# Kernel tuning notes

Hardware: AMD Instinct MI355X
Metric: run time of the kernel (lower is better)

## Reference

```python
import jax, jax.numpy as jnp
import numpy as np

N = 100000
E = 1600000
D_IN, D_EMB, D_OUT = 16, 128, 2


def _mlp(x, W1, b1, W2, b2):
    return jax.nn.relu(x @ W1 + b1) @ W2 + b2


def _gcn(x, edge_index, edge_weight, W, b):
    # PyG GCNConv: x' = W x, symmetric norm with self-loops (weight 1), scatter-add, + bias
    n = x.shape[0]
    x = x @ W
    row, col = edge_index[0], edge_index[1]
    deg = jax.ops.segment_sum(edge_weight, col, num_segments=n) + 1.0  # +1 for self-loop
    dis = jax.lax.rsqrt(deg)
    norm = dis[row] * edge_weight * dis[col]                      # [E]
    agg = jax.ops.segment_sum(norm[:, None] * x[row], col, num_segments=n)
    agg = agg + (dis * dis)[:, None] * x                          # self-loop contribution
    return agg + b


def setup_inputs() -> dict:
    key = jax.random.key(0)
    ks = jax.random.split(key, 16)
    s_in = 1.0 / np.sqrt(D_IN)
    s_emb = 1.0 / np.sqrt(D_EMB)
    return {
        "x": jax.random.normal(ks[0], (N, D_IN), dtype=jnp.float32),
        "edge_index": jax.random.randint(ks[1], (2, E), 0, N, dtype=jnp.int64),
        "edge_weight": jax.random.uniform(ks[2], (E,), dtype=jnp.float32),
        # encoder MLP
        "enc_W1": jax.random.normal(ks[3], (D_IN, D_EMB), dtype=jnp.float32) * s_in,
        "enc_b1": jnp.zeros((D_EMB,), jnp.float32),
        "enc_W2": jax.random.normal(ks[4], (D_EMB, D_EMB), dtype=jnp.float32) * s_emb,
        "enc_b2": jnp.zeros((D_EMB,), jnp.float32),
        # conv1 / conv2
        "c1_W": jax.random.normal(ks[5], (D_EMB, D_EMB), dtype=jnp.float32) * s_emb,
        "c1_b": jnp.zeros((D_EMB,), jnp.float32),
        "c2_W": jax.random.normal(ks[6], (D_EMB, D_EMB), dtype=jnp.float32) * s_emb,
        "c2_b": jnp.zeros((D_EMB,), jnp.float32),
        # decoder MLP
        "dec_W1": jax.random.normal(ks[7], (D_EMB, D_EMB), dtype=jnp.float32) * s_emb,
        "dec_b1": jnp.zeros((D_EMB,), jnp.float32),
        "dec_W2": jax.random.normal(ks[8], (D_EMB, D_OUT), dtype=jnp.float32) * s_emb,
        "dec_b2": jnp.zeros((D_OUT,), jnp.float32),
    }


def reference(x, edge_index, edge_weight,
              enc_W1, enc_b1, enc_W2, enc_b2,
              c1_W, c1_b, c2_W, c2_b,
              dec_W1, dec_b1, dec_W2, dec_b2):
    h = _mlp(x, enc_W1, enc_b1, enc_W2, enc_b2)
    h = jax.nn.relu(_gcn(h, edge_index, edge_weight, c1_W, c1_b))
    h = jax.nn.relu(_gcn(h, edge_index, edge_weight, c2_W, c2_b))
    h = _mlp(h, dec_W1, dec_b1, dec_W2, dec_b2)
    return jax.nn.softmax(h, axis=1)
```

## Files before the change

kernel.cpp:

```cpp
#include <hip/hip_runtime.h>

#define N_NODES 100000
#define N_EDGES 1600000
#define NBKT 391
#define BKT_CAP 4608
#define PART_BLOCKS 391

typedef _Float16 half8 __attribute__((ext_vector_type(8)));
typedef float floatx4 __attribute__((ext_vector_type(4)));


__global__ __launch_bounds__(256) void k_part(const int* __restrict__ ei,
                                              const float* __restrict__ ew,
                                              unsigned* __restrict__ cursor,
                                              unsigned* __restrict__ partA,
                                              float* __restrict__ partB) {
    __shared__ unsigned hist[NBKT];
    __shared__ unsigned lrank[NBKT];
    __shared__ unsigned basebuf[NBKT];
    int tid = threadIdx.x;
    int e0 = blockIdx.x * 4096 + tid * 16;
    for (int i = tid; i < NBKT; i += 256) { hist[i] = 0; lrank[i] = 0; }
    __syncthreads();

    unsigned bk[16];
    bool full = (e0 + 16 <= N_EDGES);
    if (full) {
        #pragma unroll
        for (int v = 0; v < 4; v++) {
            int4 c = *(const int4*)(ei + N_EDGES + e0 + v * 4);
            bk[v * 4 + 0] = (unsigned)c.x >> 8;
            bk[v * 4 + 1] = (unsigned)c.y >> 8;
            bk[v * 4 + 2] = (unsigned)c.z >> 8;
            bk[v * 4 + 3] = (unsigned)c.w >> 8;
        }
        #pragma unroll
        for (int i = 0; i < 16; i++) atomicAdd(&hist[bk[i]], 1u);
    } else {
        for (int i = 0; i < 16; i++) {
            if (e0 + i < N_EDGES) {
                bk[i] = (unsigned)ei[N_EDGES + e0 + i] >> 8;
                atomicAdd(&hist[bk[i]], 1u);
            }
        }
    }
    __syncthreads();
    for (int b = tid; b < NBKT; b += 256) {
        unsigned h = hist[b];
        basebuf[b] = h ? atomicAdd(&cursor[b], h) : 0u;
    }
    __syncthreads();

    if (full) {
        #pragma unroll
        for (int v = 0; v < 4; v++) {
            int4 c = *(const int4*)(ei + N_EDGES + e0 + v * 4);
            int4 r = *(const int4*)(ei + e0 + v * 4);
            float4 w = *(const float4*)(ew + e0 + v * 4);
            int cols[4] = {c.x, c.y, c.z, c.w};
            int rows[4] = {r.x, r.y, r.z, r.w};
            float ws4[4] = {w.x, w.y, w.z, w.w};
            #pragma unroll
            for (int i = 0; i < 4; i++) {
                unsigned b = bk[v * 4 + i];
                unsigned rk = atomicAdd(&lrank[b], 1u);
                size_t idx = (size_t)b * BKT_CAP + basebuf[b] + rk;
                partA[idx] = (((unsigned)cols[i] & 255u) << 17) | (unsigned)rows[i];
                partB[idx] = ws4[i];
            }
        }
    } else {
        for (int i = 0; i < 16; i++) {
            if (e0 + i < N_EDGES) {
                int col = ei[N_EDGES + e0 + i];
                int row = ei[e0 + i];
                float wv = ew[e0 + i];
                unsigned b = bk[i];
                unsigned rk = atomicAdd(&lrank[b], 1u);
                size_t idx = (size_t)b * BKT_CAP + basebuf[b] + rk;
                partA[idx] = (((unsigned)col & 255u) << 17) | (unsigned)row;
                partB[idx] = wv;
            }
        }
    }
}

__global__ __launch_bounds__(256) void k_stats(const unsigned* __restrict__ cursor,
                                               const unsigned* __restrict__ partA,
                                               const float* __restrict__ partB,
                                               float* __restrict__ dis,
                                               int* __restrict__ offs,
                                               int* __restrict__ cnt) {
    __shared__ unsigned hist[256];
    __shared__ unsigned sc[256];
    __shared__ float dacc[256];
    int tid = threadIdx.x;
    int j = blockIdx.x;
    int count = (int)cursor[j];
    size_t p0 = (size_t)j * BKT_CAP;
    hist[tid] = 0;
    dacc[tid] = 0.f;
    __syncthreads();
    for (int i = tid; i < count; i += 256) {
        unsigned a = partA[p0 + i];
        float w = partB[p0 + i];
        unsigned cl = (a >> 17) & 255u;
        atomicAdd(&hist[cl], 1u);
        atomicAdd(&dacc[cl], w);
    }
    __syncthreads();
    unsigned myc = hist[tid];
    sc[tid] = myc;
    __syncthreads();
    #pragma unroll
    for (int d = 1; d < 256; d <<= 1) {
        unsigned t = (tid >= d) ? sc[tid - d] : 0u;
        __syncthreads();
        sc[tid] += t;
        __syncthreads();
    }
    int col = j * 256 + tid;
    if (col < N_NODES) {
        dis[col] = rsqrtf(dacc[tid] + 1.0f);
        cnt[col] = (int)myc;
        offs[col] = (int)(p0 + (sc[tid] - myc));
    }
}

__global__ __launch_bounds__(256) void k_scatter(const unsigned* __restrict__ cursor,
                                                 const unsigned* __restrict__ partA,
                                                 const float* __restrict__ partB,
                                                 const int* __restrict__ offs,
                                                 const float* __restrict__ dis,
                                                 unsigned* __restrict__ csr,
                                                 float* __restrict__ svec) {
    __shared__ unsigned cur[256];
    __shared__ float sacc[256];
    int tid = threadIdx.x;
    int j = blockIdx.x;
    int count = (int)cursor[j];
    size_t p0 = (size_t)j * BKT_CAP;
    int col = j * 256 + tid;
    cur[tid] = (col < N_NODES) ? (unsigned)(offs[col] - (int)p0) : 0u;
    sacc[tid] = 0.f;
    __syncthreads();
    for (int i = tid; i < count; i += 256) {
        unsigned a = partA[p0 + i];
        float wv = partB[p0 + i];
        unsigned cl = (a >> 17) & 255u;
        unsigned row = a & 0x1FFFFu;
        unsigned r = atomicAdd(&cur[cl], 1u);
        int colg = j * 256 + (int)cl;
        float w = dis[row] * wv * dis[colg];
        _Float16 hw = (_Float16)w;
        unsigned short hb;
        __builtin_memcpy(&hb, &hw, 2);
        csr[p0 + r] = ((unsigned)hb << 17) | row;
        atomicAdd(&sacc[cl], (float)hw);
    }
    __syncthreads();
    if (col < N_NODES) {
        float d = dis[col];
        svec[col] = sacc[tid] + d * d;
    }
}

__global__ __launch_bounds__(256) void prep_mm(const float* __restrict__ W2,
                                               const float* __restrict__ c1W,
                                               _Float16* __restrict__ Wt0) {
    __shared__ float sW[128 * 128];
    int t = threadIdx.x;
    for (int i = t; i < 4096; i += 256) ((float4*)sW)[i] = ((const float4*)c1W)[i];
    __syncthreads();
    int k = blockIdx.x * 2 + (t >> 7);
    int col = t & 127;
    float acc = 0.f;
    #pragma unroll 8
    for (int j = 0; j < 128; j++) acc = fmaf(W2[k * 128 + j], sW[j * 128 + col], acc);
    Wt0[col * 128 + k] = (_Float16)acc;
}

__global__ __launch_bounds__(128) void prep_bb(const float* __restrict__ b2,
                                               const float* __restrict__ c1W,
                                               float* __restrict__ bb) {
    int c = threadIdx.x;
    float acc = 0.f;
    for (int j = 0; j < 128; j++) acc = fmaf(b2[j], c1W[j * 128 + c], acc);
    bb[c] = acc;
}

__global__ __launch_bounds__(256) void prep_tr(const float* __restrict__ Wa,
                                               const float* __restrict__ Wb,
                                               _Float16* __restrict__ Wt) {
    int m = blockIdx.x >> 4;
    const float* W = (m == 0) ? Wa : Wb;
    _Float16* o = Wt + (m + 1) * 16384;
    int base = (blockIdx.x & 15) * 1024 + threadIdx.x * 4;
    int col = base >> 7;
    int k0 = base & 127;
    #pragma unroll
    for (int i = 0; i < 4; i++) o[base + i] = (_Float16)W[(k0 + i) * 128 + col];
}


__global__ __launch_bounds__(256) void enc1_kernel(const float* __restrict__ x,
                                                   const float* __restrict__ W1,
                                                   const float* __restrict__ b1,
                                                   _Float16* __restrict__ out) {
    __shared__ float sX[256 * 17];
    __shared__ float sW[2048];
    __shared__ float sb[128];
    int t = threadIdx.x;
    int base = blockIdx.x * 256;
    for (int i = t; i < 512; i += 256) ((float4*)sW)[i] = ((const float4*)W1)[i];
    if (t < 128) sb[t] = b1[t];
    #pragma unroll
    for (int i = 0; i < 4; i++) {
        int f = i * 1024 + t * 4;
        int row = f >> 4, k = f & 15;
        float4 v = make_float4(0.f, 0.f, 0.f, 0.f);
        if (base + row < N_NODES) v = *(const float4*)(x + (size_t)(base + row) * 16 + k);
        *(float4*)(sX + row * 17 + k) = v;
    }
    __syncthreads();
    int row = base + t;
    if (row >= N_NODES) return;
    float xr[16];
    #pragma unroll
    for (int k = 0; k < 16; k++) xr[k] = sX[t * 17 + k];
    #pragma unroll 4
    for (int cb = 0; cb < 16; cb++) {
        float acc[8];
        #pragma unroll
        for (int jj = 0; jj < 8; jj++) acc[jj] = sb[cb * 8 + jj];
        #pragma unroll
        for (int k = 0; k < 16; k++) {
            float xv = xr[k];
            #pragma unroll
            for (int jj = 0; jj < 8; jj++) acc[jj] = fmaf(xv, sW[k * 128 + cb * 8 + jj], acc[jj]);
        }
        half8 h;
        #pragma unroll
        for (int jj = 0; jj < 8; jj++) h[jj] = (_Float16)fmaxf(acc[jj], 0.f);
        *(half8*)(out + (size_t)row * 128 + cb * 8) = h;
    }
}


#define GEMM_GRID 522

template <bool BIAS, bool RELU, bool DEC, bool SB>
__global__ __launch_bounds__(256, 2) void gemm_mfma(const _Float16* __restrict__ A,
                                                    const _Float16* __restrict__ Wt,
                                                    const float* __restrict__ bias,
                                                    _Float16* __restrict__ C,
                                                    const float* __restrict__ W2,
                                                    const float* __restrict__ b2,
                                                    float* __restrict__ sm_out,
                                                    const float* __restrict__ svec,
                                                    const float* __restrict__ bbv) {
    __shared__ _Float16 sA[2 * 64 * 128];
    __shared__ _Float16 sE[DEC ? 64 : 64 * 128];
    __shared__ float sW2[DEC ? 256 : 1];
    int t = threadIdx.x;
    int lane = t & 63;
    int w = t >> 6;
    int l15 = lane & 15;
    int l4 = lane >> 4;

    half8 bfrag[8][4];
    #pragma unroll
    for (int n = 0; n < 8; n++)
        #pragma unroll
        for (int kk = 0; kk < 4; kk++)
            bfrag[n][kk] = *(const half8*)(Wt + (n * 16 + l15) * 128 + kk * 32 + l4 * 8);

    float bcol[8];
    if constexpr (BIAS) {
        #pragma unroll
        for (int n = 0; n < 8; n++) bcol[n] = bias[n * 16 + l15];
    }
    float bbcol[8];
    if constexpr (SB) {
        #pragma unroll
        for (int n = 0; n < 8; n++) bbcol[n] = bbv[n * 16 + l15];
    }
    float b20 = 0.f, b21 = 0.f;
    if constexpr (DEC) {
        if (t < 256) sW2[t] = W2[t];
        b20 = b2[0]; b21 = b2[1];
    }

    auto STAGE = [&](int buf, int tile) {
        const _Float16* Ag = A + (size_t)tile * 64 * 128;
        #pragma unroll
        for (int i = 0; i < 4; i++) {
            int c = i * 256 + t;
            int row = c >> 4;
            int g = (c & 15) ^ (row & 7);
            const _Float16* src = Ag + row * 128 + g * 8;
            __builtin_amdgcn_global_load_lds(
                (const __attribute__((address_space(1))) void*)src,
                (__attribute__((address_space(3))) void*)(sA + buf * 8192 + (size_t)(i * 256 + w * 64) * 8),
                16, 0, 0);
        }
    };

    const int NT = (N_NODES + 63) / 64;
    int cur = 0;
    STAGE(0, blockIdx.x);

    for (int tile = blockIdx.x; tile < NT; tile += GEMM_GRID) {
        int nx = tile + GEMM_GRID;
        if (nx < NT) {
            STAGE(cur ^ 1, nx);
            asm volatile("s_waitcnt vmcnt(4)" ::: "memory");
        } else {
            asm volatile("s_waitcnt vmcnt(0)" ::: "memory");
        }
        __builtin_amdgcn_s_barrier();
        asm volatile("" ::: "memory");

        const _Float16* sAc = sA + cur * 8192;

        floatx4 acc[8];
        #pragma unroll
        for (int n = 0; n < 8; n++) acc[n] = (floatx4)(0.f);

        #pragma unroll
        for (int kk = 0; kk < 4; kk++) {
            int rloc = w * 16 + l15;
            int cl = kk * 4 + l4;
            int s = cl ^ (rloc & 7);
            half8 af = *(const half8*)(sAc + rloc * 128 + s * 8);
            #pragma unroll
            for (int n = 0; n < 8; n++)
                acc[n] = __builtin_amdgcn_mfma_f32_16x16x32_f16(af, bfrag[n][kk], acc[n], 0, 0, 0);
        }

        size_t base_row = (size_t)tile * 64;
        float s4[4];
        if constexpr (SB) {
            #pragma unroll
            for (int r = 0; r < 4; r++) {
                int rr = (int)base_row + w * 16 + l4 * 4 + r;
                s4[r] = (rr < N_NODES) ? svec[rr] : 0.f;
            }
        }
        if constexpr (DEC) {
            #pragma unroll
            for (int r = 0; r < 4; r++) {
                float p0 = 0.f, p1 = 0.f;
                #pragma unroll
                for (int n = 0; n < 8; n++) {
                    float v = acc[n][r];
                    if constexpr (BIAS) v += bcol[n];
                    if constexpr (RELU) v = fmaxf(v, 0.f);
                    int ch = n * 16 + l15;
                    p0 = fmaf(v, sW2[ch * 2 + 0], p0);
                    p1 = fmaf(v, sW2[ch * 2 + 1], p1);
                }
                #pragma unroll
                for (int m = 1; m < 16; m <<= 1) {
                    p0 += __shfl_xor(p0, m, 64);
                    p1 += __shfl_xor(p1, m, 64);
                }
                size_t grow = base_row + w * 16 + l4 * 4 + r;
                if (l15 == 0 && grow < N_NODES) {
                    float z0 = p0 + b20, z1 = p1 + b21;
                    float mx = fmaxf(z0, z1);
                    float e0 = expf(z0 - mx), e1 = expf(z1 - mx);
                    float si = 1.f / (e0 + e1);
                    *(float2*)(sm_out + grow * 2) = make_float2(e0 * si, e1 * si);
                }
            }
            __builtin_amdgcn_s_barrier();
            asm volatile("" ::: "memory");
        } else {
            #pragma unroll
            for (int n = 0; n < 8; n++) {
                #pragma unroll
                for (int r = 0; r < 4; r++) {
                    float v = acc[n][r];
                    if constexpr (SB) v += s4[r] * bbcol[n];
                    if constexpr (BIAS) v += bcol[n];
                    if constexpr (RELU) v = fmaxf(v, 0.f);
                    int row = w * 16 + l4 * 4 + r;
                    sE[row * 128 + n * 16 + l15] = (_Float16)v;
                }
            }
            __builtin_amdgcn_s_barrier();
            asm volatile("" ::: "memory");
            #pragma unroll
            for (int i = 0; i < 4; i++) {
                int c = i * 256 + t;
                int row = c >> 4;
                if (base_row + row < N_NODES) {
                    *(float4*)((char*)C + (base_row + row) * 256 + (c & 15) * 16) =
                        *(const float4*)((const char*)sE + (size_t)c * 16);
                }
            }
        }
        cur ^= 1;
    }
}


__global__ __launch_bounds__(256) void agg_kernel(const _Float16* __restrict__ m,
                                                  const int* __restrict__ offs,
                                                  const int* __restrict__ cnt,
                                                  const unsigned* __restrict__ csr,
                                                  const float* __restrict__ dis,
                                                  _Float16* __restrict__ out) {
    int wave = threadIdx.x >> 6;
    int lane = threadIdx.x & 63;
    int g = lane >> 4;
    int q = lane & 15;
    int j = blockIdx.x * 4 + wave;
    if (j >= N_NODES) return;
    int s = offs[j];
    int num = cnt[j];

    float acc[8];
    if (g == 0) {
        float d = dis[j];
        float dd = d * d;
        half8 mv = *(const half8*)(m + (size_t)j * 128 + q * 8);
        #pragma unroll
        for (int i = 0; i < 8; i++) acc[i] = dd * (float)mv[i];
    } else {
        #pragma unroll
        for (int i = 0; i < 8; i++) acc[i] = 0.f;
    }

    int e = 0;
    for (; e + 16 <= num; e += 16) {
        unsigned u0 = csr[s + e + g];
        unsigned u1 = csr[s + e + 4 + g];
        unsigned u2 = csr[s + e + 8 + g];
        unsigned u3 = csr[s + e + 12 + g];
        half8 r0 = *(const half8*)(m + (size_t)(u0 & 0x1FFFF) * 128 + q * 8);
        half8 r1 = *(const half8*)(m + (size_t)(u1 & 0x1FFFF) * 128 + q * 8);
        half8 r2 = *(const half8*)(m + (size_t)(u2 & 0x1FFFF) * 128 + q * 8);
        half8 r3 = *(const half8*)(m + (size_t)(u3 & 0x1FFFF) * 128 + q * 8);
        unsigned short b0 = (unsigned short)(u0 >> 17), b1 = (unsigned short)(u1 >> 17);
        unsigned short b2 = (unsigned short)(u2 >> 17), b3 = (unsigned short)(u3 >> 17);
        _Float16 h0, h1, h2, h3;
        __builtin_memcpy(&h0, &b0, 2); __builtin_memcpy(&h1, &b1, 2);
        __builtin_memcpy(&h2, &b2, 2); __builtin_memcpy(&h3, &b3, 2);
        float w0 = (float)h0, w1 = (float)h1, w2 = (float)h2, w3 = (float)h3;
        #pragma unroll
        for (int i = 0; i < 8; i++) acc[i] = fmaf(w0, (float)r0[i], acc[i]);
        #pragma unroll
        for (int i = 0; i < 8; i++) acc[i] = fmaf(w1, (float)r1[i], acc[i]);
        #pragma unroll
        for (int i = 0; i < 8; i++) acc[i] = fmaf(w2, (float)r2[i], acc[i]);
        #pragma unroll
        for (int i = 0; i < 8; i++) acc[i] = fmaf(w3, (float)r3[i], acc[i]);
    }
    for (; e < num; e += 4) {
        if (e + g < num) {
            unsigned u0 = csr[s + e + g];
            unsigned short b0 = (unsigned short)(u0 >> 17);
            _Float16 h0;
            __builtin_memcpy(&h0, &b0, 2);
            half8 r0 = *(const half8*)(m + (size_t)(u0 & 0x1FFFF) * 128 + q * 8);
            float w0 = (float)h0;
            #pragma unroll
            for (int i = 0; i < 8; i++) acc[i] = fmaf(w0, (float)r0[i], acc[i]);
        }
    }

    #pragma unroll
    for (int i = 0; i < 8; i++) {
        acc[i] += __shfl_xor(acc[i], 16, 64);
        acc[i] += __shfl_xor(acc[i], 32, 64);
    }

    if (g == 0) {
        half8 o;
        #pragma unroll
        for (int i = 0; i < 8; i++) o[i] = (_Float16)acc[i];
        *(half8*)(out + (size_t)j * 128 + q * 8) = o;
    }
}


extern "C" void kernel_launch(void* const* d_in, const int* in_sizes, int n_in,
                              void* d_out, int out_size, void* d_ws, size_t ws_size,
                              hipStream_t stream) {
    const float* x      = (const float*)d_in[0];
    const int*   ei     = (const int*)d_in[1];
    const float* ew     = (const float*)d_in[2];
    const float* enc_W1 = (const float*)d_in[3];
    const float* enc_b1 = (const float*)d_in[4];
    const float* enc_W2 = (const float*)d_in[5];
    const float* enc_b2 = (const float*)d_in[6];
    const float* c1_W   = (const float*)d_in[7];
    const float* c1_b   = (const float*)d_in[8];
    const float* c2_W   = (const float*)d_in[9];
    const float* c2_b   = (const float*)d_in[10];
    const float* dec_W1 = (const float*)d_in[11];
    const float* dec_b1 = (const float*)d_in[12];
    const float* dec_W2 = (const float*)d_in[13];
    const float* dec_b2 = (const float*)d_in[14];
    float* out = (float*)d_out;

    char* ws = (char*)d_ws;
    unsigned* partA = (unsigned*)(ws);
    float*    partB = (float*)(ws + 7206912);
    _Float16* B1 = (_Float16*)(ws);
    _Float16* B2 = (_Float16*)(ws + 25600000);
    _Float16* Wt = (_Float16*)(ws + 51200000);
    unsigned* cursor = (unsigned*)(ws + 51331072);
    float* dis     = (float*)(ws + 51333120);
    int*   offs    = (int*)  (ws + 51733120);
    int*   cnt     = (int*)  (ws + 52133120);
    unsigned* csr  = (unsigned*)(ws + 52533120);
    float* svec    = (float*)(ws + 59740032);
    float* bb      = (float*)(ws + 60140032);

    hipMemsetAsync(cursor, 0, 2048, stream);

    k_part<<<PART_BLOCKS, 256, 0, stream>>>(ei, ew, cursor, partA, partB);
    k_stats<<<NBKT, 256, 0, stream>>>(cursor, partA, partB, dis, offs, cnt);
    k_scatter<<<NBKT, 256, 0, stream>>>(cursor, partA, partB, offs, dis, csr, svec);

    prep_mm<<<64, 256, 0, stream>>>(enc_W2, c1_W, Wt);
    prep_bb<<<1, 128, 0, stream>>>(enc_b2, c1_W, bb);
    prep_tr<<<32, 256, 0, stream>>>(c2_W, dec_W1, Wt);
    enc1_kernel<<<(N_NODES + 255) / 256, 256, 0, stream>>>(x, enc_W1, enc_b1, B1);

    agg_kernel<<<N_NODES / 4, 256, 0, stream>>>(B1, offs, cnt, csr, dis, B2);
    gemm_mfma<true, true, false, true><<<GEMM_GRID, 256, 0, stream>>>(
        B2, Wt + 0 * 16384, c1_b, B1, nullptr, nullptr, nullptr, svec, bb);
    agg_kernel<<<N_NODES / 4, 256, 0, stream>>>(B1, offs, cnt, csr, dis, B2);
    gemm_mfma<true, true, false, false><<<GEMM_GRID, 256, 0, stream>>>(
        B2, Wt + 1 * 16384, c2_b, B1, nullptr, nullptr, nullptr, nullptr, nullptr);
    gemm_mfma<true, true, true, false><<<GEMM_GRID, 256, 0, stream>>>(
        B1, Wt + 2 * 16384, dec_b1, nullptr, dec_W2, dec_b2, out, nullptr, nullptr);
}
```

Measured before the change: 375.7 us.

## Retune partition and GEMM grid sizes and streamline aggregation gather loop

The partition kernel now processes half as many edges per block and launches twice as many blocks. The GEMM kernels take their tile stride from gridDim and are launched with larger grids, one of them giving each block a single tile, which spreads work over more blocks at the cost of less double-buffer prefetch reuse. The aggregation kernel drops its unrolled main loop plus remainder loop in favour of one predicated loop that clamps indices and zeroes weights for out-of-range edges. It also uses 32-bit shift/or addressing to cut index arithmetic.

```diff
diff --git a/kernel.cpp b/kernel.cpp
--- a/kernel.cpp
+++ b/kernel.cpp
@@ -4,7 +4,7 @@
 #define N_EDGES 1600000
 #define NBKT 391
 #define BKT_CAP 4608
-#define PART_BLOCKS 391
+#define PART_BLOCKS 782
 
 typedef _Float16 half8 __attribute__((ext_vector_type(8)));
 typedef float floatx4 __attribute__((ext_vector_type(4)));
@@ -19,15 +19,15 @@
     __shared__ unsigned lrank[NBKT];
     __shared__ unsigned basebuf[NBKT];
     int tid = threadIdx.x;
-    int e0 = blockIdx.x * 4096 + tid * 16;
+    int e0 = blockIdx.x * 2048 + tid * 8;
     for (int i = tid; i < NBKT; i += 256) { hist[i] = 0; lrank[i] = 0; }
     __syncthreads();
 
-    unsigned bk[16];
-    bool full = (e0 + 16 <= N_EDGES);
+    unsigned bk[8];
+    bool full = (e0 + 8 <= N_EDGES);
     if (full) {
         #pragma unroll
-        for (int v = 0; v < 4; v++) {
+        for (int v = 0; v < 2; v++) {
             int4 c = *(const int4*)(ei + N_EDGES + e0 + v * 4);
             bk[v * 4 + 0] = (unsigned)c.x >> 8;
             bk[v * 4 + 1] = (unsigned)c.y >> 8;
@@ -35,9 +35,9 @@
             bk[v * 4 + 3] = (unsigned)c.w >> 8;
         }
         #pragma unroll
-        for (int i = 0; i < 16; i++) atomicAdd(&hist[bk[i]], 1u);
+        for (int i = 0; i < 8; i++) atomicAdd(&hist[bk[i]], 1u);
     } else {
-        for (int i = 0; i < 16; i++) {
+        for (int i = 0; i < 8; i++) {
             if (e0 + i < N_EDGES) {
                 bk[i] = (unsigned)ei[N_EDGES + e0 + i] >> 8;
                 atomicAdd(&hist[bk[i]], 1u);
@@ -53,7 +53,7 @@
 
     if (full) {
         #pragma unroll
-        for (int v = 0; v < 4; v++) {
+        for (int v = 0; v < 2; v++) {
             int4 c = *(const int4*)(ei + N_EDGES + e0 + v * 4);
             int4 r = *(const int4*)(ei + e0 + v * 4);
             float4 w = *(const float4*)(ew + e0 + v * 4);
@@ -70,7 +70,7 @@
             }
         }
     } else {
-        for (int i = 0; i < 16; i++) {
+        for (int i = 0; i < 8; i++) {
             if (e0 + i < N_EDGES) {
                 int col = ei[N_EDGES + e0 + i];
                 int row = ei[e0 + i];
@@ -247,8 +247,6 @@
 }
 
 
-#define GEMM_GRID 522
-
 template <bool BIAS, bool RELU, bool DEC, bool SB>
 __global__ __launch_bounds__(256, 2) void gemm_mfma(const _Float16* __restrict__ A,
                                                     const _Float16* __restrict__ Wt,
@@ -267,6 +265,7 @@
     int w = t >> 6;
     int l15 = lane & 15;
     int l4 = lane >> 4;
+    int stride = gridDim.x;
 
     half8 bfrag[8][4];
     #pragma unroll
@@ -310,8 +309,8 @@
     int cur = 0;
     STAGE(0, blockIdx.x);
 
-    for (int tile = blockIdx.x; tile < NT; tile += GEMM_GRID) {
-        int nx = tile + GEMM_GRID;
+    for (int tile = blockIdx.x; tile < NT; tile += stride) {
+        int nx = tile + stride;
         if (nx < NT) {
             STAGE(cur ^ 1, nx);
             asm volatile("s_waitcnt vmcnt(4)" ::: "memory");
@@ -406,6 +405,13 @@
 }
 
 
+__device__ __forceinline__ float wdec(unsigned u) {
+    unsigned short b = (unsigned short)(u >> 17);
+    _Float16 h;
+    __builtin_memcpy(&h, &b, 2);
+    return (float)h;
+}
+
 __global__ __launch_bounds__(256) void agg_kernel(const _Float16* __restrict__ m,
                                                   const int* __restrict__ offs,
                                                   const int* __restrict__ cnt,
@@ -420,12 +426,13 @@
     if (j >= N_NODES) return;
     int s = offs[j];
     int num = cnt[j];
+    unsigned qoff = (unsigned)(q * 8);
 
     float acc[8];
     if (g == 0) {
         float d = dis[j];
         float dd = d * d;
-        half8 mv = *(const half8*)(m + (size_t)j * 128 + q * 8);
+        half8 mv = *(const half8*)(m + (((unsigned)j << 7) | qoff));
         #pragma unroll
         for (int i = 0; i < 8; i++) acc[i] = dd * (float)mv[i];
     } else {
@@ -433,42 +440,29 @@
         for (int i = 0; i < 8; i++) acc[i] = 0.f;
     }
 
-    int e = 0;
-    for (; e + 16 <= num; e += 16) {
-        unsigned u0 = csr[s + e + g];
-        unsigned u1 = csr[s + e + 4 + g];
-        unsigned u2 = csr[s + e + 8 + g];
-        unsigned u3 = csr[s + e + 12 + g];
-        half8 r0 = *(const half8*)(m + (size_t)(u0 & 0x1FFFF) * 128 + q * 8);
-        half8 r1 = *(const half8*)(m + (size_t)(u1 & 0x1FFFF) * 128 + q * 8);
-        half8 r2 = *(const half8*)(m + (size_t)(u2 & 0x1FFFF) * 128 + q * 8);
-        half8 r3 = *(const half8*)(m + (size_t)(u3 & 0x1FFFF) * 128 + q * 8);
-        unsigned short b0 = (unsigned short)(u0 >> 17), b1 = (unsigned short)(u1 >> 17);
-        unsigned short b2 = (unsigned short)(u2 >> 17), b3 = (unsigned short)(u3 >> 17);
-        _Float16 h0, h1, h2, h3;
-        __builtin_memcpy(&h0, &b0, 2); __builtin_memcpy(&h1, &b1, 2);
-        __builtin_memcpy(&h2, &b2, 2); __builtin_memcpy(&h3, &b3, 2);
-        float w0 = (float)h0, w1 = (float)h1, w2 = (float)h2, w3 = (float)h3;
-        #pragma unroll
-        for (int i = 0; i < 8; i++) acc[i] = fmaf(w0, (float)r0[i], acc[i]);
-        #pragma unroll
-        for (int i = 0; i < 8; i++) acc[i] = fmaf(w1, (float)r1[i], acc[i]);
-        #pragma unroll
-        for (int i = 0; i < 8; i++) acc[i] = fmaf(w2, (float)r2[i], acc[i]);
-        #pragma unroll
-        for (int i = 0; i < 8; i++) acc[i] = fmaf(w3, (float)r3[i], acc[i]);
-    }
-    for (; e < num; e += 4) {
-        if (e + g < num) {
-            unsigned u0 = csr[s + e + g];
-            unsigned short b0 = (unsigned short)(u0 >> 17);
-            _Float16 h0;
-            __builtin_memcpy(&h0, &b0, 2);
-            half8 r0 = *(const half8*)(m + (size_t)(u0 & 0x1FFFF) * 128 + q * 8);
-            float w0 = (float)h0;
-            #pragma unroll
-            for (int i = 0; i < 8; i++) acc[i] = fmaf(w0, (float)r0[i], acc[i]);
-        }
+    for (int e = 0; e < num; e += 16) {
+        float wv[4];
+        unsigned off[4];
+        #pragma unroll
+        for (int k = 0; k < 4; k++) {
+            int idx = e + k * 4 + g;
+            int idc = (idx < num) ? idx : (num - 1);
+            unsigned uu = csr[s + idc];
+            wv[k] = (idx < num) ? wdec(uu) : 0.f;
+            off[k] = ((uu & 0x1FFFFu) << 7) | qoff;
+        }
+        half8 r0 = *(const half8*)(m + off[0]);
+        half8 r1 = *(const half8*)(m + off[1]);
+        half8 r2 = *(const half8*)(m + off[2]);
+        half8 r3 = *(const half8*)(m + off[3]);
+        #pragma unroll
+        for (int i = 0; i < 8; i++) acc[i] = fmaf(wv[0], (float)r0[i], acc[i]);
+        #pragma unroll
+        for (int i = 0; i < 8; i++) acc[i] = fmaf(wv[1], (float)r1[i], acc[i]);
+        #pragma unroll
+        for (int i = 0; i < 8; i++) acc[i] = fmaf(wv[2], (float)r2[i], acc[i]);
+        #pragma unroll
+        for (int i = 0; i < 8; i++) acc[i] = fmaf(wv[3], (float)r3[i], acc[i]);
     }
 
     #pragma unroll
@@ -481,7 +475,7 @@
         half8 o;
         #pragma unroll
         for (int i = 0; i < 8; i++) o[i] = (_Float16)acc[i];
-        *(half8*)(out + (size_t)j * 128 + q * 8) = o;
+        *(half8*)(out + (((unsigned)j << 7) | qoff)) = o;
     }
 }
 
@@ -532,11 +526,11 @@
     enc1_kernel<<<(N_NODES + 255) / 256, 256, 0, stream>>>(x, enc_W1, enc_b1, B1);
 
     agg_kernel<<<N_NODES / 4, 256, 0, stream>>>(B1, offs, cnt, csr, dis, B2);
-    gemm_mfma<true, true, false, true><<<GEMM_GRID, 256, 0, stream>>>(
+    gemm_mfma<true, true, false, true><<<781, 256, 0, stream>>>(
         B2, Wt + 0 * 16384, c1_b, B1, nullptr, nullptr, nullptr, svec, bb);
     agg_kernel<<<N_NODES / 4, 256, 0, stream>>>(B1, offs, cnt, csr, dis, B2);
-    gemm_mfma<true, true, false, false><<<GEMM_GRID, 256, 0, stream>>>(
+    gemm_mfma<true, true, false, false><<<781, 256, 0, stream>>>(
         B2, Wt + 1 * 16384, c2_b, B1, nullptr, nullptr, nullptr, nullptr, nullptr);
-    gemm_mfma<true, true, true, false><<<GEMM_GRID, 256, 0, stream>>>(
+    gemm_mfma<true, true, true, false><<<1563, 256, 0, stream>>>(
         B1, Wt + 2 * 16384, dec_b1, nullptr, dec_W2, dec_b2, out, nullptr, nullptr);
 }
```

Result: slower. 392.2 us (+4.4%).
